# Kernel tuning notes

Hardware: AMD Instinct MI355X
Metric: run time of the kernel (lower is better)

Reference implementation:

```python
import jax, jax.numpy as jnp
import numpy as np

M, N, H, C = 50000, 50000, 32, 128
K, GROUPS = 15, 8
CPG = C // GROUPS           # 16, channels per group
RADIUS, SIGMA, INF = 2.5, 1.0, 1.0e6
EPS = 1e-5                  # GroupNorm eps
NEG_SLOPE = 0.1             # LeakyReLU slope in alpha MLP


def setup_inputs() -> dict:
    key = jax.random.key(0)
    ks = jax.random.split(key, 12)
    q_pts = jax.random.normal(ks[0], (M, 3), jnp.float32) * 5.0
    s_pts = q_pts  # same-resolution layer: q == s
    s_feats = jax.random.normal(ks[1], (N, C), jnp.float32)
    neighb_inds = jax.random.randint(ks[2], (M, H), 0, N + 1)  # N = padding index
    # kernel points: center + 14 points in a sphere of given radius
    kp = jax.random.normal(ks[3], (K, 3), jnp.float32)
    kp = kp / (jnp.linalg.norm(kp, axis=1, keepdims=True) + 1e-9) * RADIUS * 0.66
    k_pts = kp.at[0].set(0.0)
    # alpha MLP: Linear(C->C) + LeakyReLU + Linear(C->K*CPG)
    W1 = jax.random.normal(ks[4], (C, C), jnp.float32) * np.sqrt(2.0 / C)
    b1 = jnp.zeros((C,), jnp.float32)
    W2 = jax.random.normal(ks[5], (C, K * CPG), jnp.float32) * np.sqrt(2.0 / C)
    b2 = jnp.zeros((K * CPG,), jnp.float32)
    gn_w = jnp.ones((K * CPG,), jnp.float32)
    gn_b = jnp.zeros((K * CPG,), jnp.float32)
    return {"q_pts": q_pts, "s_pts": s_pts, "s_feats": s_feats,
            "neighb_inds": neighb_inds, "k_pts": k_pts,
            "W1": W1, "b1": b1, "W2": W2, "b2": b2,
            "gn_w": gn_w, "gn_b": gn_b}


def reference(q_pts, s_pts, s_feats, k_pts, W1, b1, W2, b2, gn_w, gn_b, neighb_inds):
    m = q_pts.shape[0]
    # ---- neighbor geometry (no_grad in original) ----
    s_pts_pad = jnp.concatenate([s_pts, jnp.full((1, 3), INF, s_pts.dtype)], 0)
    neighbors = s_pts_pad[neighb_inds] - q_pts[:, None, :]          # (M,H,3)
    sq = jnp.sum((neighbors[:, :, None, :] - k_pts) ** 2, -1)       # (M,H,K)
    nn_sq = jnp.min(sq, -1)                                         # (M,H)
    nn_1nn = jnp.argmin(sq, -1)                                     # (M,H)
    infl = jnp.clip(1.0 - jnp.sqrt(nn_sq) / SIGMA, 0.0)             # linear influence
    # ---- neighbor features gather (padding row = zeros) ----
    feats_pad = jnp.concatenate([s_feats, jnp.zeros((1, C), s_feats.dtype)], 0)
    neighbor_feats = feats_pad[neighb_inds]                         # (M,H,C)
    # ---- dynamic weights from center features (q==s -> pooled = s_feats) ----
    pooled = s_feats
    h = pooled @ W1 + b1
    h = jnp.where(h >= 0, h, NEG_SLOPE * h)                         # LeakyReLU(0.1)
    cw = (h @ W2 + b2).reshape(m, K, CPG)                           # (M,K,CPG)
    # GroupNorm(K groups over K*CPG channels), stats over (points, CPG) per group
    mu = jnp.mean(cw, axis=(0, 2), keepdims=True)
    var = jnp.var(cw, axis=(0, 2), keepdims=True)
    cw = (cw - mu) * jax.lax.rsqrt(var + EPS)
    cw = cw * gn_w.reshape(1, K, CPG) + gn_b.reshape(1, K, CPG)
    # ---- gather weights at nearest kernel point, modulate by influence ----
    nw = jnp.take_along_axis(cw, nn_1nn[:, :, None], axis=1)        # (M,H,CPG)
    nw = nw * infl[:, :, None]                                      # weight_act = identity
    # ---- multiply and sum over neighbors ----
    nf = neighbor_feats.reshape(m, H, CPG, GROUPS)
    out = jnp.sum(nf * nw[:, :, :, None], axis=1)                   # (M,CPG,GROUPS)
    return out.reshape(m, C)
```

## Files before the change

kernel.cpp:

```cpp
#include <hip/hip_runtime.h>
#include <hip/hip_bf16.h>

#define Mpts 50000
#define Npts 50000
#define Hn 32
#define Cc 128
#define Kk 15
#define NCW 240

typedef __attribute__((ext_vector_type(8))) short short8;
typedef __attribute__((ext_vector_type(4))) float f32x4;
typedef __attribute__((ext_vector_type(2))) float f32x2;
typedef unsigned int u32;

__device__ inline ushort f2bf(float f) {
  __hip_bfloat16 h = __float2bfloat16(f);
  return *reinterpret_cast<ushort*>(&h);
}

__global__ __launch_bounds__(256) void k0_pre(
    const float* __restrict__ q_pts, const float* __restrict__ s_pts,
    const int* __restrict__ nb, const float* __restrict__ kp,
    const float* __restrict__ W1, const float* __restrict__ W2,
    ushort* __restrict__ sfb, ushort* __restrict__ W1t,
    ushort* __restrict__ W2t, float* __restrict__ stats,
    u32* __restrict__ geomP)
{
  const int t = threadIdx.x;
  const int b = blockIdx.x;
  if (b < 6250) {
    __shared__ float kpt[3][15];
    if (t < 45) kpt[t % 3][t / 3] = kp[t];
    __syncthreads();
    const int gtid = b * 256 + t;
    const int m = gtid >> 5;
    int idx = nb[gtid]; if (idx > Npts) idx = Npts;
    float qx = q_pts[m * 3 + 0], qy = q_pts[m * 3 + 1], qz = q_pts[m * 3 + 2];
    float px, py, pz;
    if (idx < Npts) { px = s_pts[idx * 3 + 0]; py = s_pts[idx * 3 + 1]; pz = s_pts[idx * 3 + 2]; }
    else            { px = 1.0e6f; py = 1.0e6f; pz = 1.0e6f; }
    float nx = px - qx, ny = py - qy, nz = pz - qz;
    int ksel = 0; float best = 1e30f;
#pragma unroll
    for (int k = 0; k < Kk; ++k) {
      float dx = nx - kpt[0][k], dy = ny - kpt[1][k], dz = nz - kpt[2][k];
      float d = dx * dx + dy * dy + dz * dz;
      if (d < best) { best = d; ksel = k; }
    }
    float infl = 1.f - sqrtf(best);
    infl = infl > 0.f ? infl : 0.f;
    geomP[gtid] = (__float_as_uint(infl) & 0xFFFFFFF0u) | (u32)ksel;
  } else if (b < 6252) {
    __shared__ ushort TT[240][66];
    const int k0 = (b - 6250) * 64;
#pragma unroll
    for (int i = 0; i < 32; ++i) {
      int e = t + i * 256;
      int r = e >> 7, c = e & 127;
      TT[c][r] = f2bf(W1[(size_t)(k0 + r) * Cc + c]);
    }
    __syncthreads();
    int n = t >> 1, half = t & 1;
    union { short8 v[4]; ushort u[32]; } pk;
#pragma unroll
    for (int i = 0; i < 32; ++i) pk.u[i] = TT[n][half * 32 + i];
#pragma unroll
    for (int q = 0; q < 4; ++q)
      *(short8*)(W1t + (size_t)n * Cc + k0 + half * 32 + q * 8) = pk.v[q];
  } else if (b < 6254) {
    __shared__ ushort TT[240][66];
    const int k0 = (b - 6252) * 64;
    for (int i = 0; i < 60; ++i) {
      int e = t + i * 256;
      int r = e / 240, c = e % 240;
      TT[c][r] = f2bf(W2[(size_t)(k0 + r) * NCW + c]);
    }
    __syncthreads();
    if (t < 240) {
      union { short8 v[8]; ushort u[64]; } pk;
#pragma unroll
      for (int i = 0; i < 64; ++i) pk.u[i] = TT[t][i];
#pragma unroll
      for (int q = 0; q < 8; ++q)
        *(short8*)(W2t + (size_t)t * Cc + k0 + q * 8) = pk.v[q];
    }
  } else {
    if (t < 16) {
      short8 z = short8{0,0,0,0,0,0,0,0};
      *(short8*)(sfb + (size_t)Npts * Cc + t * 8) = z;
    }
    if (t < 128) {
      float4 z4 = make_float4(0.f, 0.f, 0.f, 0.f);
      *(float4*)(stats + t * 4) = z4;
    }
  }
}

__global__ __launch_bounds__(256, 3) void k1_mlp(
    const float* __restrict__ sfeat, const ushort* __restrict__ W1t,
    const float* __restrict__ b1, const ushort* __restrict__ W2t,
    const float* __restrict__ b2, ushort* __restrict__ sfb,
    ushort* __restrict__ cw, float* __restrict__ stats)
{
  __shared__ __align__(16) ushort shA[64 * 128];
  __shared__ __align__(16) ushort shW[128 * 128];
  __shared__ float red[2][15][4];

  const int t = threadIdx.x;
  const int r0 = blockIdx.x * 64;
  const int wid = t >> 6, lane = t & 63;
  const int l16 = lane & 15, lq = lane >> 4;

  float4 fA[4], fB[4];
#pragma unroll
  for (int p = 0; p < 4; ++p) {
    int id = p * 256 + t;
    int r = id >> 4, c = id & 15;
    int g = r0 + r;
    fA[p] = make_float4(0.f, 0.f, 0.f, 0.f);
    fB[p] = make_float4(0.f, 0.f, 0.f, 0.f);
    if (g < Mpts) {
      const float* src = sfeat + (size_t)g * Cc + c * 8;
      fA[p] = *(const float4*)(src);
      fB[p] = *(const float4*)(src + 4);
    }
  }
  uint4 wv[8];
#pragma unroll
  for (int p = 0; p < 8; ++p) {
    int id = p * 256 + t;
    int r = id >> 4, c = id & 15;
    wv[p] = *(const uint4*)(W1t + r * Cc + c * 8);
  }
  asm volatile("" :: "v"(wv[0].x), "v"(wv[1].x), "v"(wv[2].x), "v"(wv[3].x),
                     "v"(wv[4].x), "v"(wv[5].x), "v"(wv[6].x), "v"(wv[7].x),
                     "v"(fA[0].x), "v"(fA[1].x), "v"(fA[2].x), "v"(fA[3].x),
                     "v"(fB[0].x), "v"(fB[1].x), "v"(fB[2].x), "v"(fB[3].x));
#pragma unroll
  for (int p = 0; p < 8; ++p) {
    int id = p * 256 + t;
    int r = id >> 4, c = id & 15;
    *(uint4*)((char*)shW + ((r * 256 + c * 16) ^ ((r & 7) << 4))) = wv[p];
  }
#pragma unroll
  for (int p = 0; p < 4; ++p) {
    int id = p * 256 + t;
    int r = id >> 4, c = id & 15;
    int g = r0 + r;
    union { short8 s; ushort u[8]; } pk;
    pk.u[0] = f2bf(fA[p].x); pk.u[1] = f2bf(fA[p].y); pk.u[2] = f2bf(fA[p].z); pk.u[3] = f2bf(fA[p].w);
    pk.u[4] = f2bf(fB[p].x); pk.u[5] = f2bf(fB[p].y); pk.u[6] = f2bf(fB[p].z); pk.u[7] = f2bf(fB[p].w);
    if (g < Mpts) *(short8*)(sfb + (size_t)g * Cc + c * 8) = pk.s;
    *(short8*)((char*)shA + ((r * 256 + c * 16) ^ ((r & 7) << 4))) = pk.s;
  }
  __syncthreads();

  const int arow = wid * 16 + l16;
  const int axor = (arow & 7) << 4;

  f32x4 acc1[8];
#pragma unroll
  for (int nt = 0; nt < 8; ++nt) acc1[nt] = f32x4{0.f, 0.f, 0.f, 0.f};
#pragma unroll
  for (int kt = 0; kt < 4; ++kt) {
    const int koff2 = (kt * 32 + lq * 8) * 2;
    short8 a = *(const short8*)((const char*)shA + ((arow * 256 + koff2) ^ axor));
#pragma unroll
    for (int nt = 0; nt < 8; ++nt) {
      int wrow = nt * 16 + l16;
      short8 b = *(const short8*)((const char*)shW + ((wrow * 256 + koff2) ^ ((wrow & 7) << 4)));
      acc1[nt] = __builtin_amdgcn_mfma_f32_16x16x32_bf16(a, b, acc1[nt], 0, 0, 0);
    }
  }
#pragma unroll
  for (int nt = 0; nt < 8; ++nt) {
    int col = nt * 16 + l16;
    float bias = b1[col];
#pragma unroll
    for (int reg = 0; reg < 4; ++reg) {
      float h = acc1[nt][reg] + bias;
      h = h >= 0.f ? h : 0.1f * h;
      int row = wid * 16 + lq * 4 + reg;
      int byte = ((row * 256) + col * 2) ^ ((row & 7) << 4);
      *(ushort*)((char*)shA + byte) = f2bf(h);
    }
  }

  f32x4 acc2[8], acc3[7];
#pragma unroll
  for (int j = 0; j < 8; ++j) acc2[j] = f32x4{0.f, 0.f, 0.f, 0.f};
#pragma unroll
  for (int j = 0; j < 7; ++j) acc3[j] = f32x4{0.f, 0.f, 0.f, 0.f};

  __syncthreads();
  {
    uint4 wv2[8];
#pragma unroll
    for (int p = 0; p < 8; ++p) {
      int id = p * 256 + t;
      int r = id >> 4, c = id & 15;
      wv2[p] = *(const uint4*)(W2t + (size_t)r * Cc + c * 8);
    }
    asm volatile("" :: "v"(wv2[0].x), "v"(wv2[1].x), "v"(wv2[2].x), "v"(wv2[3].x),
                       "v"(wv2[4].x), "v"(wv2[5].x), "v"(wv2[6].x), "v"(wv2[7].x));
#pragma unroll
    for (int p = 0; p < 8; ++p) {
      int id = p * 256 + t;
      int r = id >> 4, c = id & 15;
      *(uint4*)((char*)shW + ((r * 256 + c * 16) ^ ((r & 7) << 4))) = wv2[p];
    }
  }
  __syncthreads();
#pragma unroll
  for (int kt = 0; kt < 4; ++kt) {
    const int koff2 = (kt * 32 + lq * 8) * 2;
    short8 a = *(const short8*)((const char*)shA + ((arow * 256 + koff2) ^ axor));
#pragma unroll
    for (int j = 0; j < 8; ++j) {
      int wrow = j * 16 + l16;
      short8 b = *(const short8*)((const char*)shW + ((wrow * 256 + koff2) ^ ((wrow & 7) << 4)));
      acc2[j] = __builtin_amdgcn_mfma_f32_16x16x32_bf16(a, b, acc2[j], 0, 0, 0);
    }
  }

  __syncthreads();
  {
    uint4 wv2[7];
#pragma unroll
    for (int p = 0; p < 7; ++p) {
      int id = p * 256 + t;
      int r = id >> 4, c = id & 15;
      wv2[p] = *(const uint4*)(W2t + (size_t)(128 + r) * Cc + c * 8);
    }
    asm volatile("" :: "v"(wv2[0].x), "v"(wv2[1].x), "v"(wv2[2].x), "v"(wv2[3].x),
                       "v"(wv2[4].x), "v"(wv2[5].x), "v"(wv2[6].x));
#pragma unroll
    for (int p = 0; p < 7; ++p) {
      int id = p * 256 + t;
      int r = id >> 4, c = id & 15;
      *(uint4*)((char*)shW + ((r * 256 + c * 16) ^ ((r & 7) << 4))) = wv2[p];
    }
  }
  __syncthreads();
#pragma unroll
  for (int kt = 0; kt < 4; ++kt) {
    const int koff2 = (kt * 32 + lq * 8) * 2;
    short8 a = *(const short8*)((const char*)shA + ((arow * 256 + koff2) ^ axor));
#pragma unroll
    for (int j = 0; j < 7; ++j) {
      int wrow = j * 16 + l16;
      short8 b = *(const short8*)((const char*)shW + ((wrow * 256 + koff2) ^ ((wrow & 7) << 4)));
      acc3[j] = __builtin_amdgcn_mfma_f32_16x16x32_bf16(a, b, acc3[j], 0, 0, 0);
    }
  }
  __syncthreads();

  ushort* shB = shW;
  float s[15], ss[15];
#pragma unroll
  for (int j = 0; j < 15; ++j) { s[j] = 0.f; ss[j] = 0.f; }
  const int rowb = wid * 16 + lq * 4;
#pragma unroll
  for (int j = 0; j < 15; ++j) {
    int col = j * 16 + l16;
    float bias = b2[col];
#pragma unroll
    for (int reg = 0; reg < 4; ++reg) {
      float v = (j < 8 ? acc2[j][reg] : acc3[j - 8][reg]) + bias;
      shB[(rowb + reg) * 244 + col] = f2bf(v);
      if (r0 + rowb + reg < Mpts) { s[j] += v; ss[j] += v * v; }
    }
  }
  __syncthreads();

  {
    char* cwB = (char*)cw + (size_t)r0 * 480;
#pragma unroll
    for (int i = 0; i < 8; ++i) {
      int gid = i * 256 + t;
      if (gid < 1920) {
        int row = gid / 30;
        int rem = (gid - row * 30) * 16;
        if (r0 + row < Mpts) {
          uint4 v = *(const uint4*)((const char*)shB + row * 488 + rem);
          *(uint4*)(cwB + (size_t)row * 480 + rem) = v;
        }
      }
    }
  }

#pragma unroll
  for (int j = 0; j < 15; ++j) {
    for (int off = 32; off > 0; off >>= 1) {
      s[j]  += __shfl_xor(s[j],  off);
      ss[j] += __shfl_xor(ss[j], off);
    }
  }
  if (lane == 0) {
#pragma unroll
    for (int j = 0; j < 15; ++j) { red[0][j][wid] = s[j]; red[1][j][wid] = ss[j]; }
  }
  __syncthreads();
  float* st = stats + (blockIdx.x & 7) * 64;
  if (t < 15) {
    float S = red[0][t][0] + red[0][t][1] + red[0][t][2] + red[0][t][3];
    atomicAdd(&st[t], S);
  } else if (t >= 32 && t < 47) {
    int j = t - 32;
    float SS = red[1][j][0] + red[1][j][1] + red[1][j][2] + red[1][j][3];
    atomicAdd(&st[32 + j], SS);
  }
}

__global__ __launch_bounds__(256) void k3_out(
    const ushort* __restrict__ sfb, const int* __restrict__ nb,
    const u32* __restrict__ geomP, const float* __restrict__ gn_w,
    const float* __restrict__ gn_b, const float* __restrict__ stats,
    const ushort* __restrict__ cw, float* __restrict__ out)
{
  __shared__ float Atab[255], Btab[255];
  __shared__ float mus[16], rss[16];
  __shared__ float wtab[4][2][8][33];
  const int t = threadIdx.x;

  if (t < 15) {
    float S = 0.f, SS = 0.f;
#pragma unroll
    for (int r = 0; r < 8; ++r) { S += stats[r * 64 + t]; SS += stats[r * 64 + 32 + t]; }
    const float inv = 1.0f / (16.0f * (float)Mpts);
    float mu = S * inv;
    float var = SS * inv - mu * mu;
    mus[t] = mu;
    rss[t] = rsqrtf(var + 1e-5f);
  }
  __syncthreads();
  if (t < 240) {
    int k = t >> 4, c = t & 15;
    float a = rss[k] * gn_w[t];
    Atab[k * 17 + c] = a;
    Btab[k * 17 + c] = gn_b[t] - mus[k] * a;
  }
  __syncthreads();

  const int half = (blockIdx.x >= 6250) ? 1 : 0;
  const int pblk = blockIdx.x - half * 6250;
  const int wid = t >> 6, lane = t & 63;
  const int mbase = pblk * 8 + wid * 2;
  const int gtid = pblk * 256 + t;
  const int ch = lane & 7, hlane = (lane >> 3) & 3, p = lane >> 5;
  const int half8 = half * 8;

  u32 g = geomP[gtid];
  int idxv = nb[gtid]; if (idxv > Npts) idxv = Npts;

  int ih[8];
#pragma unroll
  for (int j = 0; j < 8; ++j)
    ih[j] = __shfl(idxv, (p << 5) | (hlane + 4 * j));

  {
    int h = lane >> 1, c0 = (lane & 1) * 4;
#pragma unroll
    for (int q = 0; q < 2; ++q) {
      u32 gp = __shfl((int)g, (q << 5) | h);
      int kh = gp & 15;
      float wI = __uint_as_float(gp & 0xFFFFFFF0u);
      uint2 cwv = *(const uint2*)(cw + (size_t)(mbase + q) * NCW + kh * 16 + half8 + c0);
      const float* Ar = &Atab[kh * 17 + half8 + c0];
      const float* Br = &Btab[kh * 17 + half8 + c0];
      float v0 = __uint_as_float(cwv.x << 16);
      float v1 = __uint_as_float(cwv.x & 0xffff0000u);
      float v2 = __uint_as_float(cwv.y << 16);
      float v3 = __uint_as_float(cwv.y & 0xffff0000u);
      wtab[wid][q][c0 + 0][h] = fmaf(v0, Ar[0], Br[0]) * wI;
      wtab[wid][q][c0 + 1][h] = fmaf(v1, Ar[1], Br[1]) * wI;
      wtab[wid][q][c0 + 2][h] = fmaf(v2, Ar[2], Br[2]) * wI;
      wtab[wid][q][c0 + 3][h] = fmaf(v3, Ar[3], Br[3]) * wI;
    }
  }

  const uint4* fb = (const uint4*)sfb;
  f32x2 a0 = {0.f, 0.f}, a1 = {0.f, 0.f}, a2 = {0.f, 0.f}, a3 = {0.f, 0.f};

#pragma unroll
  for (int ph = 0; ph < 2; ++ph) {
    const int lo = ph * 25000, hi = lo + 25000;
    uint4 fv[8];
#pragma unroll
    for (int j = 0; j < 8; ++j) {
      int e = ih[j];
      int addr = (e >= lo && e < hi) ? e : Npts;
      fv[j] = fb[addr * 16 + half8 + ch];
    }
    asm volatile("" :: "v"(fv[0].x), "v"(fv[1].x), "v"(fv[2].x), "v"(fv[3].x),
                       "v"(fv[4].x), "v"(fv[5].x), "v"(fv[6].x), "v"(fv[7].x));
#pragma unroll
    for (int j = 0; j < 8; ++j) {
      if (ih[j] >= lo && ih[j] < hi) {
        float w = wtab[wid][p][ch][hlane + 4 * j];
        f32x2 w2 = {w, w};
        u32 ux = fv[j].x, uy = fv[j].y, uz = fv[j].z, uw = fv[j].w;
        f32x2 q0 = {__uint_as_float(ux << 16), __uint_as_float(ux & 0xffff0000u)};
        f32x2 q1 = {__uint_as_float(uy << 16), __uint_as_float(uy & 0xffff0000u)};
        f32x2 q2 = {__uint_as_float(uz << 16), __uint_as_float(uz & 0xffff0000u)};
        f32x2 q3 = {__uint_as_float(uw << 16), __uint_as_float(uw & 0xffff0000u)};
        a0 = __builtin_elementwise_fma(q0, w2, a0);
        a1 = __builtin_elementwise_fma(q1, w2, a1);
        a2 = __builtin_elementwise_fma(q2, w2, a2);
        a3 = __builtin_elementwise_fma(q3, w2, a3);
      }
    }
  }

#pragma unroll
  for (int off = 8; off <= 16; off <<= 1) {
    a0[0] += __shfl_xor(a0[0], off); a0[1] += __shfl_xor(a0[1], off);
    a1[0] += __shfl_xor(a1[0], off); a1[1] += __shfl_xor(a1[1], off);
    a2[0] += __shfl_xor(a2[0], off); a2[1] += __shfl_xor(a2[1], off);
    a3[0] += __shfl_xor(a3[0], off); a3[1] += __shfl_xor(a3[1], off);
  }
  if ((lane & 24) == 0) {
    float* op = out + (size_t)(mbase + p) * Cc + half * 64 + ch * 8;
    float4 o0; o0.x = a0[0]; o0.y = a0[1]; o0.z = a1[0]; o0.w = a1[1];
    float4 o1; o1.x = a2[0]; o1.y = a2[1]; o1.z = a3[0]; o1.w = a3[1];
    *(float4*)(op)     = o0;
    *(float4*)(op + 4) = o1;
  }
}

extern "C" void kernel_launch(void* const* d_in, const int* in_sizes, int n_in,
                              void* d_out, int out_size, void* d_ws, size_t ws_size,
                              hipStream_t stream) {
  const float* q_pts  = (const float*)d_in[0];
  const float* s_pts  = (const float*)d_in[1];
  const float* sfeat  = (const float*)d_in[2];
  const int*   nb     = (const int*)d_in[3];
  const float* kp     = (const float*)d_in[4];
  const float* W1     = (const float*)d_in[5];
  const float* b1     = (const float*)d_in[6];
  const float* W2     = (const float*)d_in[7];
  const float* b2     = (const float*)d_in[8];
  const float* gn_w   = (const float*)d_in[9];
  const float* gn_b   = (const float*)d_in[10];
  float* out   = (float*)d_out;

  char* wsb = (char*)d_ws;
  float*  stats = (float*)wsb;
  ushort* sfb   = (ushort*)(wsb + 4096);
  ushort* W1t   = (ushort*)(wsb + 12804352);
  ushort* W2t   = (ushort*)(wsb + 12837120);
  ushort* cwb   = (ushort*)(wsb + 12898560);
  u32*    geomP = (u32*)   (wsb + 36898560);

  k0_pre<<<6255, 256, 0, stream>>>(q_pts, s_pts, nb, kp, W1, W2,
                                   sfb, W1t, W2t, stats, geomP);
  k1_mlp<<<(Mpts + 63) / 64, 256, 0, stream>>>(sfeat, W1t, b1, W2t, b2,
                                               sfb, cwb, stats);
  k3_out<<<12500, 256, 0, stream>>>(sfb, nb, geomP, gn_w, gn_b, stats,
                                    cwb, out);
}
```

Measured before the change: 115.0 us.

## Fuse neighbor geometry into output kernel and drop two-phase feature gather

Moves the nearest-kernel-point and influence computation out of the preprocessing kernel and into the output kernel, so the packed geometry buffer is no longer written and read through global memory. The preprocessing launch shrinks to a handful of blocks that only transpose weights. The output kernel also replaces its two-phase, index-range-partitioned feature gather with a single gather of all 8 neighbor rows, issued before the geometry math so the loads overlap it. In exchange, the geometry work is now done twice, once per channel-half block, and the locality the range split was meant to provide is lost.

Result: faster. 108.6 us (-5.5%).

```diff
diff --git a/kernel.cpp b/kernel.cpp
--- a/kernel.cpp
+++ b/kernel.cpp
@@ -19,40 +19,15 @@
 }
 
 __global__ __launch_bounds__(256) void k0_pre(
-    const float* __restrict__ q_pts, const float* __restrict__ s_pts,
-    const int* __restrict__ nb, const float* __restrict__ kp,
     const float* __restrict__ W1, const float* __restrict__ W2,
     ushort* __restrict__ sfb, ushort* __restrict__ W1t,
-    ushort* __restrict__ W2t, float* __restrict__ stats,
-    u32* __restrict__ geomP)
+    ushort* __restrict__ W2t, float* __restrict__ stats)
 {
+  __shared__ ushort TT[240][66];
   const int t = threadIdx.x;
   const int b = blockIdx.x;
-  if (b < 6250) {
-    __shared__ float kpt[3][15];
-    if (t < 45) kpt[t % 3][t / 3] = kp[t];
-    __syncthreads();
-    const int gtid = b * 256 + t;
-    const int m = gtid >> 5;
-    int idx = nb[gtid]; if (idx > Npts) idx = Npts;
-    float qx = q_pts[m * 3 + 0], qy = q_pts[m * 3 + 1], qz = q_pts[m * 3 + 2];
-    float px, py, pz;
-    if (idx < Npts) { px = s_pts[idx * 3 + 0]; py = s_pts[idx * 3 + 1]; pz = s_pts[idx * 3 + 2]; }
-    else            { px = 1.0e6f; py = 1.0e6f; pz = 1.0e6f; }
-    float nx = px - qx, ny = py - qy, nz = pz - qz;
-    int ksel = 0; float best = 1e30f;
-#pragma unroll
-    for (int k = 0; k < Kk; ++k) {
-      float dx = nx - kpt[0][k], dy = ny - kpt[1][k], dz = nz - kpt[2][k];
-      float d = dx * dx + dy * dy + dz * dz;
-      if (d < best) { best = d; ksel = k; }
-    }
-    float infl = 1.f - sqrtf(best);
-    infl = infl > 0.f ? infl : 0.f;
-    geomP[gtid] = (__float_as_uint(infl) & 0xFFFFFFF0u) | (u32)ksel;
-  } else if (b < 6252) {
-    __shared__ ushort TT[240][66];
-    const int k0 = (b - 6250) * 64;
+  if (b < 2) {
+    const int k0 = b * 64;
 #pragma unroll
     for (int i = 0; i < 32; ++i) {
       int e = t + i * 256;
@@ -67,9 +42,8 @@
 #pragma unroll
     for (int q = 0; q < 4; ++q)
       *(short8*)(W1t + (size_t)n * Cc + k0 + half * 32 + q * 8) = pk.v[q];
-  } else if (b < 6254) {
-    __shared__ ushort TT[240][66];
-    const int k0 = (b - 6252) * 64;
+  } else if (b < 4) {
+    const int k0 = (b - 2) * 64;
     for (int i = 0; i < 60; ++i) {
       int e = t + i * 256;
       int r = e / 240, c = e % 240;
@@ -313,13 +287,15 @@
 }
 
 __global__ __launch_bounds__(256) void k3_out(
+    const float* __restrict__ q_pts, const float* __restrict__ s_pts,
     const ushort* __restrict__ sfb, const int* __restrict__ nb,
-    const u32* __restrict__ geomP, const float* __restrict__ gn_w,
+    const float* __restrict__ kp, const float* __restrict__ gn_w,
     const float* __restrict__ gn_b, const float* __restrict__ stats,
     const ushort* __restrict__ cw, float* __restrict__ out)
 {
   __shared__ float Atab[255], Btab[255];
   __shared__ float mus[16], rss[16];
+  __shared__ float kpt[3][15];
   __shared__ float wtab[4][2][8][33];
   const int t = threadIdx.x;
 
@@ -332,6 +308,9 @@
     float var = SS * inv - mu * mu;
     mus[t] = mu;
     rss[t] = rsqrtf(var + 1e-5f);
+  } else if (t >= 64 && t < 109) {
+    int i = t - 64;
+    kpt[i % 3][i / 3] = kp[i];
   }
   __syncthreads();
   if (t < 240) {
@@ -350,19 +329,43 @@
   const int ch = lane & 7, hlane = (lane >> 3) & 3, p = lane >> 5;
   const int half8 = half * 8;
 
-  u32 g = geomP[gtid];
   int idxv = nb[gtid]; if (idxv > Npts) idxv = Npts;
 
   int ih[8];
 #pragma unroll
   for (int j = 0; j < 8; ++j)
     ih[j] = __shfl(idxv, (p << 5) | (hlane + 4 * j));
+  const uint4* fb = (const uint4*)sfb;
+  uint4 fv[8];
+#pragma unroll
+  for (int j = 0; j < 8; ++j)
+    fv[j] = fb[ih[j] * 16 + half8 + ch];
+
+  u32 gpk;
+  {
+    const int mg = mbase + (lane >> 5);
+    float qx = q_pts[mg * 3 + 0], qy = q_pts[mg * 3 + 1], qz = q_pts[mg * 3 + 2];
+    float px, py, pz;
+    if (idxv < Npts) { px = s_pts[idxv * 3 + 0]; py = s_pts[idxv * 3 + 1]; pz = s_pts[idxv * 3 + 2]; }
+    else             { px = 1.0e6f; py = 1.0e6f; pz = 1.0e6f; }
+    float nx = px - qx, ny = py - qy, nz = pz - qz;
+    int ksel = 0; float best = 1e30f;
+#pragma unroll
+    for (int k = 0; k < Kk; ++k) {
+      float dx = nx - kpt[0][k], dy = ny - kpt[1][k], dz = nz - kpt[2][k];
+      float d = dx * dx + dy * dy + dz * dz;
+      if (d < best) { best = d; ksel = k; }
+    }
+    float infl = 1.f - sqrtf(best);
+    infl = infl > 0.f ? infl : 0.f;
+    gpk = (__float_as_uint(infl) & 0xFFFFFFF0u) | (u32)ksel;
+  }
 
   {
     int h = lane >> 1, c0 = (lane & 1) * 4;
 #pragma unroll
     for (int q = 0; q < 2; ++q) {
-      u32 gp = __shfl((int)g, (q << 5) | h);
+      u32 gp = __shfl((int)gpk, (q << 5) | h);
       int kh = gp & 15;
       float wI = __uint_as_float(gp & 0xFFFFFFF0u);
       uint2 cwv = *(const uint2*)(cw + (size_t)(mbase + q) * NCW + kh * 16 + half8 + c0);
@@ -379,39 +382,24 @@
     }
   }
 
-  const uint4* fb = (const uint4*)sfb;
+  asm volatile("" :: "v"(fv[0].x), "v"(fv[1].x), "v"(fv[2].x), "v"(fv[3].x),
+                     "v"(fv[4].x), "v"(fv[5].x), "v"(fv[6].x), "v"(fv[7].x));
+
   f32x2 a0 = {0.f, 0.f}, a1 = {0.f, 0.f}, a2 = {0.f, 0.f}, a3 = {0.f, 0.f};
-
-#pragma unroll
-  for (int ph = 0; ph < 2; ++ph) {
-    const int lo = ph * 25000, hi = lo + 25000;
-    uint4 fv[8];
-#pragma unroll
-    for (int j = 0; j < 8; ++j) {
-      int e = ih[j];
-      int addr = (e >= lo && e < hi) ? e : Npts;
-      fv[j] = fb[addr * 16 + half8 + ch];
-    }
-    asm volatile("" :: "v"(fv[0].x), "v"(fv[1].x), "v"(fv[2].x), "v"(fv[3].x),
-                       "v"(fv[4].x), "v"(fv[5].x), "v"(fv[6].x), "v"(fv[7].x));
-#pragma unroll
-    for (int j = 0; j < 8; ++j) {
-      if (ih[j] >= lo && ih[j] < hi) {
-        float w = wtab[wid][p][ch][hlane + 4 * j];
-        f32x2 w2 = {w, w};
-        u32 ux = fv[j].x, uy = fv[j].y, uz = fv[j].z, uw = fv[j].w;
-        f32x2 q0 = {__uint_as_float(ux << 16), __uint_as_float(ux & 0xffff0000u)};
-        f32x2 q1 = {__uint_as_float(uy << 16), __uint_as_float(uy & 0xffff0000u)};
-        f32x2 q2 = {__uint_as_float(uz << 16), __uint_as_float(uz & 0xffff0000u)};
-        f32x2 q3 = {__uint_as_float(uw << 16), __uint_as_float(uw & 0xffff0000u)};
-        a0 = __builtin_elementwise_fma(q0, w2, a0);
-        a1 = __builtin_elementwise_fma(q1, w2, a1);
-        a2 = __builtin_elementwise_fma(q2, w2, a2);
-        a3 = __builtin_elementwise_fma(q3, w2, a3);
-      }
-    }
-  }
-
+#pragma unroll
+  for (int j = 0; j < 8; ++j) {
+    float w = wtab[wid][p][ch][hlane + 4 * j];
+    f32x2 w2 = {w, w};
+    u32 ux = fv[j].x, uy = fv[j].y, uz = fv[j].z, uw = fv[j].w;
+    f32x2 q0 = {__uint_as_float(ux << 16), __uint_as_float(ux & 0xffff0000u)};
+    f32x2 q1 = {__uint_as_float(uy << 16), __uint_as_float(uy & 0xffff0000u)};
+    f32x2 q2 = {__uint_as_float(uz << 16), __uint_as_float(uz & 0xffff0000u)};
+    f32x2 q3 = {__uint_as_float(uw << 16), __uint_as_float(uw & 0xffff0000u)};
+    a0 = __builtin_elementwise_fma(q0, w2, a0);
+    a1 = __builtin_elementwise_fma(q1, w2, a1);
+    a2 = __builtin_elementwise_fma(q2, w2, a2);
+    a3 = __builtin_elementwise_fma(q3, w2, a3);
+  }
 #pragma unroll
   for (int off = 8; off <= 16; off <<= 1) {
     a0[0] += __shfl_xor(a0[0], off); a0[1] += __shfl_xor(a0[1], off);
@@ -450,12 +438,10 @@
   ushort* W1t   = (ushort*)(wsb + 12804352);
   ushort* W2t   = (ushort*)(wsb + 12837120);
   ushort* cwb   = (ushort*)(wsb + 12898560);
-  u32*    geomP = (u32*)   (wsb + 36898560);
-
-  k0_pre<<<6255, 256, 0, stream>>>(q_pts, s_pts, nb, kp, W1, W2,
-                                   sfb, W1t, W2t, stats, geomP);
+
+  k0_pre<<<5, 256, 0, stream>>>(W1, W2, sfb, W1t, W2t, stats);
   k1_mlp<<<(Mpts + 63) / 64, 256, 0, stream>>>(sfeat, W1t, b1, W2t, b2,
                                                sfb, cwb, stats);
-  k3_out<<<12500, 256, 0, stream>>>(sfb, nb, geomP, gn_w, gn_b, stats,
-                                    cwb, out);
+  k3_out<<<12500, 256, 0, stream>>>(q_pts, s_pts, sfb, nb, kp, gn_w, gn_b,
+                                    stats, cwb, out);
 }
```
